# Optimization experiments

Hardware: AMD Instinct MI355X
Metric: run time of the kernel (lower is better)

The kernel has to match this reference:

```python
import jax, jax.numpy as jnp
import numpy as np

DIM = 384
HEADS = 6
POINTS = 4
LEVELS = 3
FFN_DIM = 1024
EPS = 1e-6
SHAPES = [(128, 128), (64, 64), (32, 32)]  # (H, W) per level
B = 4
NQ = 4096


def layer_norm(x, g, b):
    m = jnp.mean(x, axis=-1, keepdims=True)
    v = jnp.mean(jnp.square(x - m), axis=-1, keepdims=True)
    return (x - m) * jax.lax.rsqrt(v + EPS) * g + b


def _bilinear_sample(vl, loc, h, w):
    # vl: [B, heads, Dh, h*w] per-level value; loc: [B, Nq, heads, P, 2] in [0,1]
    # grid_sample(align_corners=False, padding_mode='zeros') semantics
    Bn, Hh, Dh, _ = vl.shape
    Nq, P = loc.shape[1], loc.shape[3]
    x = loc[..., 0] * w - 0.5
    y = loc[..., 1] * h - 0.5
    x0 = jnp.floor(x); y0 = jnp.floor(y)
    wx1 = x - x0; wx0 = 1.0 - wx1
    wy1 = y - y0; wy0 = 1.0 - wy1
    acc = jnp.zeros((Bn, Hh, Dh, Nq, P), dtype=vl.dtype)
    for xi, yi, wgt in ((x0, y0, wx0 * wy0), (x0 + 1, y0, wx1 * wy0),
                        (x0, y0 + 1, wx0 * wy1), (x0 + 1, y0 + 1, wx1 * wy1)):
        valid = (xi >= 0) & (xi <= w - 1) & (yi >= 0) & (yi <= h - 1)
        idx = (jnp.clip(yi, 0, h - 1) * w + jnp.clip(xi, 0, w - 1)).astype(jnp.int32)
        idx = idx.transpose(0, 2, 1, 3).reshape(Bn, Hh, 1, Nq * P)  # [B,heads,1,Nq*P]
        g = jnp.take_along_axis(vl, jnp.broadcast_to(idx, (Bn, Hh, Dh, Nq * P)), axis=3)
        g = g.reshape(Bn, Hh, Dh, Nq, P)
        wm = (wgt * valid.astype(wgt.dtype)).transpose(0, 2, 1, 3)[:, :, None]  # [B,heads,1,Nq,P]
        acc = acc + g * wm
    return acc  # [B, heads, Dh, Nq, P]


def msda(query, value, reference_points, shapes_np, W_off, b_off, W_aw, b_aw, W_v, b_v, W_o, b_o):
    Bn, Nq, D = query.shape
    L = len(shapes_np)
    Dh = D // HEADS
    v = value @ W_v.T + b_v  # [B, Nv, D]
    offsets = (query @ W_off.T + b_off).reshape(Bn, Nq, HEADS, L, POINTS, 2)
    aw = (query @ W_aw.T + b_aw).reshape(Bn, Nq, HEADS, L * POINTS)
    aw = jax.nn.softmax(aw, axis=-1).reshape(Bn, Nq, HEADS, L, POINTS)
    # offset normalizer is [W, H] per level
    norm = jnp.asarray([[w, h] for (h, w) in shapes_np], dtype=query.dtype)
    loc = reference_points[:, :, None, :, None, :] + offsets / norm[None, None, None, :, None, :]
    out = jnp.zeros((Bn, Nq, HEADS, Dh), dtype=query.dtype)
    start = 0
    for l, (h, w) in enumerate(shapes_np):
        vl = v[:, start:start + h * w].reshape(Bn, h * w, HEADS, Dh)
        vl = vl.transpose(0, 2, 3, 1)  # [B, heads, Dh, h*w]
        sampled = _bilinear_sample(vl, loc[:, :, :, l], h, w)  # [B,heads,Dh,Nq,P]
        out = out + jnp.einsum('bhdqp,bqhp->bqhd', sampled, aw[:, :, :, l])
        start += h * w
    return out.reshape(Bn, Nq, D) @ W_o.T + b_o


def setup_inputs():
    key = jax.random.key(0)
    ks = jax.random.split(key, 16)
    nv = sum(h * w for h, w in SHAPES)
    s = 0.02
    f32 = jnp.float32
    return dict(
        query=jax.random.normal(ks[0], (B, NQ, DIM), f32),
        reference_points=jax.random.uniform(ks[1], (B, NQ, LEVELS, 2), f32),
        feat=jax.random.normal(ks[2], (B, nv, DIM), f32),
        spatial_shapes=jnp.asarray(SHAPES, jnp.int32),
        level_start_index=jnp.asarray(np.cumsum([0] + [h * w for h, w in SHAPES])[:-1], jnp.int32),
        qn_g=jnp.ones((DIM,), f32), qn_b=jnp.zeros((DIM,), f32),
        fn_g=jnp.ones((DIM,), f32), fn_b=jnp.zeros((DIM,), f32),
        W_off=jax.random.normal(ks[3], (HEADS * LEVELS * POINTS * 2, DIM), f32) * s,
        b_off=jax.random.normal(ks[4], (HEADS * LEVELS * POINTS * 2,), f32) * s,
        W_aw=jax.random.normal(ks[5], (HEADS * LEVELS * POINTS, DIM), f32) * s,
        b_aw=jnp.zeros((HEADS * LEVELS * POINTS,), f32),
        W_v=jax.random.normal(ks[6], (DIM, DIM), f32) * s, b_v=jnp.zeros((DIM,), f32),
        W_o=jax.random.normal(ks[7], (DIM, DIM), f32) * s, b_o=jnp.zeros((DIM,), f32),
        n1_g=jnp.ones((DIM,), f32), n1_b=jnp.zeros((DIM,), f32),
        W1=jax.random.normal(ks[8], (FFN_DIM, DIM), f32) * s, b1=jnp.zeros((FFN_DIM,), f32),
        W2=jax.random.normal(ks[9], (DIM, FFN_DIM), f32) * s, b2=jnp.zeros((DIM,), f32),
        n2_g=jnp.ones((DIM,), f32), n2_b=jnp.zeros((DIM,), f32),
        gamma=jnp.full((DIM,), 0.01, f32),
    )


def reference(query, reference_points, feat, spatial_shapes, level_start_index,
              qn_g, qn_b, fn_g, fn_b,
              W_off, b_off, W_aw, b_aw, W_v, b_v, W_o, b_o,
              n1_g, n1_b, W1, b1, W2, b2, n2_g, n2_b, gamma):
    shapes_np = [tuple(int(v) for v in row) for row in np.asarray(spatial_shapes)]
    qn = layer_norm(query, qn_g, qn_b)
    fn = layer_norm(feat, fn_g, fn_b)
    # cross_attn (mmcv MSDeformAttn adds identity=query internally, dropout=0)
    x = qn + msda(qn, fn, reference_points, shapes_np,
                  W_off, b_off, W_aw, b_aw, W_v, b_v, W_o, b_o)
    x = layer_norm(x, n1_g, n1_b)
    x = x + (jax.nn.gelu(x @ W1.T + b1) @ W2.T + b2)  # FFN with residual
    x = layer_norm(x, n2_g, n2_b)
    return query + gamma * x
```

## Files before the change

### kernel.cpp

```cpp
#include <hip/hip_runtime.h>
#include <hip/hip_bf16.h>

#define DIMD 384
#define HEADS 6
#define DH 64
#define LEVELS 3
#define POINTS 4
#define FFN 1024
#define BB 4
#define NQ 4096
#define NV 21504
#define MQ (BB*NQ)
#define MV (BB*NV)
#define EPSF 1e-6f

typedef __hip_bfloat16 bf16;
typedef __attribute__((ext_vector_type(8))) short bf16x8;
typedef __attribute__((ext_vector_type(4))) float f32x4;

__device__ __forceinline__ float wave_sum(float v){
  #pragma unroll
  for(int o=32;o;o>>=1) v += __shfl_xor(v,o);
  return v;
}

__global__ __launch_bounds__(256) void prep_k(
  const float* __restrict__ Wv, const float* __restrict__ Wo,
  const float* __restrict__ W1, const float* __restrict__ W2,
  const float* __restrict__ Woff, const float* __restrict__ Waw,
  const float* __restrict__ boff, const float* __restrict__ baw,
  bf16* __restrict__ wv, bf16* __restrict__ wo, bf16* __restrict__ w1,
  bf16* __restrict__ w2, bf16* __restrict__ wcat, float* __restrict__ bcat)
{
  int i = blockIdx.x*256 + threadIdx.x;
  if(i < 147456){ wv[i] = __float2bfloat16(Wv[i]); return; }
  i -= 147456;
  if(i < 147456){ wo[i] = __float2bfloat16(Wo[i]); return; }
  i -= 147456;
  if(i < 393216){ w1[i] = __float2bfloat16(W1[i]); return; }
  i -= 393216;
  if(i < 393216){ w2[i] = __float2bfloat16(W2[i]); return; }
  i -= 393216;
  if(i < 98304){
    int r = i/384, c = i - r*384;
    float v = r<144 ? Woff[r*384+c] : (r<216 ? Waw[(r-144)*384+c] : 0.f);
    wcat[i] = __float2bfloat16(v); return;
  }
  i -= 98304;
  if(i < 256){ bcat[i] = i<144 ? boff[i] : (i<216 ? baw[i-144] : 0.f); }
}

template<int INBF,int OUTBF,int FINAL>
__global__ __launch_bounds__(256) void ln_k(const void* __restrict__ xv,
    const float* __restrict__ g, const float* __restrict__ b,
    const float* __restrict__ q, const float* __restrict__ gamma,
    void* __restrict__ outv, int nrows)
{
  int row = blockIdx.x*4 + (threadIdx.x>>6);
  int lane = threadIdx.x & 63;
  if(row >= nrows) return;
  float vals[6];
  float s=0.f, s2=0.f;
  #pragma unroll
  for(int i=0;i<6;i++){
    float v;
    if constexpr(INBF) v = __bfloat162float(((const bf16*)xv)[(size_t)row*DIMD + lane + i*64]);
    else               v = ((const float*)xv)[(size_t)row*DIMD + lane + i*64];
    vals[i]=v; s += v; s2 += v*v;
  }
  s = wave_sum(s); s2 = wave_sum(s2);
  float m = s*(1.f/DIMD);
  float var = s2*(1.f/DIMD) - m*m;
  float r = rsqrtf(var + EPSF);
  #pragma unroll
  for(int i=0;i<6;i++){
    int k = lane + i*64;
    float t = (vals[i]-m)*r*g[k] + b[k];
    if constexpr(FINAL){
      t = q[(size_t)row*DIMD + k] + gamma[k]*t;
      ((float*)outv)[(size_t)row*DIMD + k] = t;
    } else if constexpr(OUTBF){
      ((bf16*)outv)[(size_t)row*DIMD + k] = __float2bfloat16(t);
    } else {
      ((float*)outv)[(size_t)row*DIMD + k] = t;
    }
  }
}

__global__ __launch_bounds__(512,4) void vgemm_k(
    const bf16* __restrict__ A, const bf16* __restrict__ Bw,
    const float* __restrict__ bias, bf16* __restrict__ out)
{
  __shared__ __align__(16) short As[64*64];
  __shared__ __align__(16) short Bs[384*64];
  const int tid = threadIdx.x;
  const int wid = tid>>6, lane = tid&63;
  const int m0 = blockIdx.x*64;
  f32x4 acc[4][3] = {};
  const int lr8 = lane>>3;
  const int lc8 = (lane&7)*8;

  for(int k0=0; k0<DIMD; k0+=64){
    {
      const bf16* srcA = A + (size_t)(m0 + wid*8 + lr8)*DIMD + k0 + lc8;
      __builtin_amdgcn_global_load_lds((const __attribute__((address_space(1))) void*)srcA,
          (__attribute__((address_space(3))) void*)(As + wid*512), 16, 0, 0);
    }
    #pragma unroll
    for(int u=0;u<6;u++){
      const int t = wid*6 + u;
      const bf16* srcB = Bw + (size_t)(t*8 + lr8)*DIMD + k0 + lc8;
      __builtin_amdgcn_global_load_lds((const __attribute__((address_space(1))) void*)srcB,
          (__attribute__((address_space(3))) void*)(Bs + t*512), 16, 0, 0);
    }
    asm volatile("s_waitcnt vmcnt(0)" ::: "memory");
    __syncthreads();
    #pragma unroll
    for(int ks=0;ks<2;ks++){
      const int cbase = ks*32 + (lane>>4)*8;
      bf16x8 af[4], bfr[3];
      #pragma unroll
      for(int i=0;i<4;i++){
        const int ar = i*16 + (lane&15);
        af[i] = *(const bf16x8*)(As + ar*64 + cbase);
      }
      #pragma unroll
      for(int j=0;j<3;j++){
        const int br = wid*48 + j*16 + (lane&15);
        bfr[j] = *(const bf16x8*)(Bs + br*64 + cbase);
      }
      #pragma unroll
      for(int i=0;i<4;i++)
        #pragma unroll
        for(int j=0;j<3;j++)
          acc[i][j] = __builtin_amdgcn_mfma_f32_16x16x32_bf16(af[i], bfr[j], acc[i][j], 0,0,0);
    }
    __syncthreads();
  }
  #pragma unroll
  for(int i=0;i<4;i++){
    const int r0 = m0 + i*16 + (lane>>4)*4;
    #pragma unroll
    for(int j=0;j<3;j++){
      const int col = wid*48 + j*16 + (lane&15);
      const float bv = bias[col];
      #pragma unroll
      for(int rr=0;rr<4;rr++)
        out[(size_t)(r0+rr)*DIMD + col] = __float2bfloat16(acc[i][j][rr] + bv);
    }
  }
}

template<int GELU_,int STBF,int RES>
__global__ __launch_bounds__(256) void mgemm_k(
    const bf16* __restrict__ A, const bf16* __restrict__ Bw,
    const float* __restrict__ bias, const bf16* __restrict__ res,
    void* __restrict__ Cv, int M, int K, int Nreal, int ldc)
{
  __shared__ __align__(16) short As[128*64];
  __shared__ __align__(16) short Bs[128*64];
  const int tid  = threadIdx.x;
  const int wid  = tid>>6, lane = tid&63;
  const int wr   = wid>>1, wc = wid&1;
  const int m0   = blockIdx.y*128, n0 = blockIdx.x*128;
  f32x4 acc[4][4] = {};

  const int sr = (lane>>3);
  const int sc = (lane&7)*8;

  for(int k0=0; k0<K; k0+=64){
    #pragma unroll
    for(int u=0;u<4;u++){
      const int t = wid*4 + u;
      const int r = t*8 + sr;
      const bf16* srcA = A  + (size_t)(m0+r)*K + k0 + sc;
      const bf16* srcB = Bw + (size_t)(n0+r)*K + k0 + sc;
      __builtin_amdgcn_global_load_lds((const __attribute__((address_space(1))) void*)srcA,
          (__attribute__((address_space(3))) void*)(As + t*512), 16, 0, 0);
      __builtin_amdgcn_global_load_lds((const __attribute__((address_space(1))) void*)srcB,
          (__attribute__((address_space(3))) void*)(Bs + t*512), 16, 0, 0);
    }
    asm volatile("s_waitcnt vmcnt(0)" ::: "memory");
    __syncthreads();
    #pragma unroll
    for(int ks=0;ks<2;ks++){
      bf16x8 af[4], bfr[4];
      #pragma unroll
      for(int i=0;i<4;i++){
        const int ar = wr*64 + i*16 + (lane&15);
        af[i]  = *(const bf16x8*)(As + ar*64 + ks*32 + (lane>>4)*8);
        const int br = wc*64 + i*16 + (lane&15);
        bfr[i] = *(const bf16x8*)(Bs + br*64 + ks*32 + (lane>>4)*8);
      }
      #pragma unroll
      for(int i=0;i<4;i++)
        #pragma unroll
        for(int j=0;j<4;j++)
          acc[i][j] = __builtin_amdgcn_mfma_f32_16x16x32_bf16(af[i], bfr[j], acc[i][j], 0,0,0);
    }
    __syncthreads();
  }
  #pragma unroll
  for(int i=0;i<4;i++){
    const int rbase = m0 + wr*64 + i*16 + (lane>>4)*4;
    #pragma unroll
    for(int j=0;j<4;j++){
      const int col = n0 + wc*64 + j*16 + (lane&15);
      if(col >= Nreal) continue;
      const float bv = bias[col];
      #pragma unroll
      for(int rr=0;rr<4;rr++){
        const int rowg = rbase + rr;
        float v = acc[i][j][rr] + bv;
        if constexpr(RES) v += __bfloat162float(res[(size_t)rowg*ldc + col]);
        if constexpr(GELU_){ float u=v; v = 0.5f*u*(1.f+tanhf(0.7978845608028654f*(u+0.044715f*u*u*u))); }
        if constexpr(STBF) ((bf16*)Cv)[(size_t)rowg*ldc + col] = __float2bfloat16(v);
        else               ((float*)Cv)[(size_t)rowg*ldc + col] = v;
      }
    }
  }
}

__global__ __launch_bounds__(256) void msda_k(
    const bf16* __restrict__ v, const float* __restrict__ offaw,
    const float* __restrict__ refp, const int* __restrict__ sshapes,
    const int* __restrict__ lstart, bf16* __restrict__ out)
{
  __shared__ uint2 plds[8][48];
  const int pid0 = blockIdx.x*8;
  const int tid = threadIdx.x;
  if(tid < 96){
    const int pl = tid/12, p12 = tid - pl*12;
    const int pid = pid0 + pl;
    const int bq = pid/6, h = pid - bq*6;
    const int b  = bq >> 12;
    const float* row = offaw + (size_t)bq*216;
    float mx = -1e30f;
    #pragma unroll
    for(int i=0;i<12;i++) mx = fmaxf(mx, row[144 + h*12 + i]);
    float ssum = 0.f, my = 0.f;
    #pragma unroll
    for(int i=0;i<12;i++){
      const float e = __expf(row[144 + h*12 + i] - mx);
      ssum += e;
      if(i==p12) my = e;
    }
    const float aww = my/ssum;
    const int l = p12>>2, pp = p12&3;
    const int hh = sshapes[2*l], ww = sshapes[2*l+1];
    const int st = lstart[l];
    const float rx = refp[((size_t)bq*LEVELS + l)*2 + 0];
    const float ry = refp[((size_t)bq*LEVELS + l)*2 + 1];
    const float ox = row[(h*12 + p12)*2 + 0];
    const float oy = row[(h*12 + p12)*2 + 1];
    const float px = (rx + ox/(float)ww)*(float)ww - 0.5f;
    const float py = (ry + oy/(float)hh)*(float)hh - 0.5f;
    const float fx0 = floorf(px), fy0 = floorf(py);
    const int x0 = (int)fx0, y0 = (int)fy0;
    const float wx1 = px - fx0, wx0 = 1.f - wx1;
    const float wy1 = py - fy0, wy0 = 1.f - wy1;
    #pragma unroll
    for(int c=0;c<4;c++){
      const int xi = x0 + (c&1);
      const int yi = y0 + (c>>1);
      const float wgt = (c&1 ? wx1 : wx0) * (c>>1 ? wy1 : wy0);
      const bool valid = (xi>=0) & (xi<=ww-1) & (yi>=0) & (yi<=hh-1);
      const int cx = min(max(xi,0), ww-1);
      const int cy = min(max(yi,0), hh-1);
      const unsigned off = (unsigned)((((b*NV + st + cy*ww + cx)*DIMD) + h*DH)*2);
      uint2 pr; pr.x = off; pr.y = __float_as_uint(valid ? wgt*aww : 0.f);
      plds[pl][p12*4 + c] = pr;
    }
  }
  __syncthreads();
  const int pl  = (tid>>5);
  const int pid = pid0 + pl;
  const int ch  = tid & 31;
  const char* vb = (const char*)v;
  float a0 = 0.f, a1 = 0.f;
  #pragma unroll
  for(int c=0;c<48;c++){
    const uint2 pr = plds[pl][c];
    const unsigned g = *(const unsigned*)(vb + pr.x + (ch<<2));
    const float w = __uint_as_float(pr.y);
    a0 = fmaf(w, __uint_as_float(g << 16), a0);
    a1 = fmaf(w, __uint_as_float(g & 0xffff0000u), a1);
  }
  const int bq = pid/6, h = pid - bq*6;
  const unsigned u0 = (unsigned)__builtin_bit_cast(unsigned short, __float2bfloat16(a0));
  const unsigned u1 = (unsigned)__builtin_bit_cast(unsigned short, __float2bfloat16(a1));
  *(unsigned*)((char*)out + (size_t)bq*768 + h*128 + (ch<<2)) = u0 | (u1<<16);
}

static inline size_t rnd(size_t x){ return (x + 511) & ~(size_t)511; }

extern "C" void kernel_launch(void* const* d_in, const int* in_sizes, int n_in,
                              void* d_out, int out_size, void* d_ws, size_t ws_size,
                              hipStream_t stream)
{
  const float* query = (const float*)d_in[0];
  const float* refp  = (const float*)d_in[1];
  const float* feat  = (const float*)d_in[2];
  const int*   sshp  = (const int*)d_in[3];
  const int*   lst   = (const int*)d_in[4];
  const float* qn_g  = (const float*)d_in[5];
  const float* qn_b  = (const float*)d_in[6];
  const float* fn_g  = (const float*)d_in[7];
  const float* fn_b  = (const float*)d_in[8];
  const float* W_off = (const float*)d_in[9];
  const float* b_off = (const float*)d_in[10];
  const float* W_aw  = (const float*)d_in[11];
  const float* b_aw  = (const float*)d_in[12];
  const float* W_v   = (const float*)d_in[13];
  const float* b_v   = (const float*)d_in[14];
  const float* W_o   = (const float*)d_in[15];
  const float* b_o   = (const float*)d_in[16];
  const float* n1_g  = (const float*)d_in[17];
  const float* n1_b  = (const float*)d_in[18];
  const float* W1    = (const float*)d_in[19];
  const float* b1    = (const float*)d_in[20];
  const float* W2    = (const float*)d_in[21];
  const float* b2    = (const float*)d_in[22];
  const float* n2_g  = (const float*)d_in[23];
  const float* n2_b  = (const float*)d_in[24];
  const float* gam   = (const float*)d_in[25];

  char* p = (char*)d_ws;
  bf16* featn = (bf16*)p;
  char* late  = p;
  p += rnd((size_t)MV*DIMD*2);
  bf16* vbuf  = (bf16*)p;  p += rnd((size_t)MV*DIMD*2);
  bf16* qn    = (bf16*)p;  p += rnd((size_t)MQ*DIMD*2);
  bf16* wv    = (bf16*)p;  p += rnd((size_t)147456*2);
  bf16* wo    = (bf16*)p;  p += rnd((size_t)147456*2);
  bf16* w1    = (bf16*)p;  p += rnd((size_t)393216*2);
  bf16* w2    = (bf16*)p;  p += rnd((size_t)393216*2);
  bf16* wcat  = (bf16*)p;  p += rnd((size_t)98304*2);
  float* bcat = (float*)p; p += rnd((size_t)256*4);
  bf16* hbuf  = (bf16*)p;  p += rnd((size_t)MQ*FFN*2);
  bf16* ybuf  = (bf16*)p;  p += rnd((size_t)MQ*DIMD*2);
  char* q2 = late;
  float* offaw = (float*)q2; q2 += rnd((size_t)MQ*216*4);
  bf16*  msda  = (bf16*)q2;  q2 += rnd((size_t)MQ*DIMD*2);
  bf16*  x1    = (bf16*)q2;  q2 += rnd((size_t)MQ*DIMD*2);
  bf16*  x2    = (bf16*)q2;  q2 += rnd((size_t)MQ*DIMD*2);

  prep_k<<<4609, 256, 0, stream>>>(W_v, W_o, W1, W2, W_off, W_aw, b_off, b_aw,
                                   wv, wo, w1, w2, wcat, bcat);
  ln_k<0,1,0><<<MV/4, 256, 0, stream>>>(feat, fn_g, fn_b, nullptr, nullptr, featn, MV);
  ln_k<0,1,0><<<MQ/4, 256, 0, stream>>>(query, qn_g, qn_b, nullptr, nullptr, qn, MQ);
  vgemm_k<<<MV/64, 512, 0, stream>>>(featn, wv, b_v, vbuf);
  mgemm_k<0,0,0><<<dim3(2, MQ/128), 256, 0, stream>>>(qn, wcat, bcat, nullptr, offaw,
                                                      MQ, DIMD, 216, 216);
  msda_k<<<MQ*HEADS/8, 256, 0, stream>>>(vbuf, offaw, refp, sshp, lst, msda);
  mgemm_k<0,1,1><<<dim3(3, MQ/128), 256, 0, stream>>>(msda, wo, b_o, qn, x1,
                                                      MQ, DIMD, DIMD, DIMD);
  ln_k<1,1,0><<<MQ/4, 256, 0, stream>>>(x1, n1_g, n1_b, nullptr, nullptr, x2, MQ);
  mgemm_k<1,1,0><<<dim3(8, MQ/128), 256, 0, stream>>>(x2, w1, b1, nullptr, hbuf,
                                                      MQ, DIMD, FFN, FFN);
  mgemm_k<0,1,1><<<dim3(3, MQ/128), 256, 0, stream>>>(hbuf, w2, b2, x2, ybuf,
                                                      MQ, FFN, DIMD, DIMD);
  ln_k<1,0,1><<<MQ/4, 256, 0, stream>>>(ybuf, n2_g, n2_b, query, gam, (float*)d_out, MQ);
}
```

Baseline: 266.2 us.

## Fuse feature LayerNorm into value-projection GEMM

Replaces the separate LayerNorm pass over the feature map and the value GEMM with one kernel. Each 32-row tile loads its fp32 rows into LDS, normalises them and writes bf16 rows back to LDS, then multiplies by the full 384-column W_v. This avoids writing and re-reading the normalised feature buffer in global memory. In exchange, the tile shrinks to 32 rows with 256 threads and uses about 72KB of dynamic LDS, which lowers occupancy and means W_v is reloaded by twice as many blocks.

Result: slower. 273.2 us (+2.6%).

```diff
diff --git a/kernel.cpp b/kernel.cpp
--- a/kernel.cpp
+++ b/kernel.cpp
@@ -87,29 +87,64 @@
   }
 }
 
-__global__ __launch_bounds__(512,4) void vgemm_k(
-    const bf16* __restrict__ A, const bf16* __restrict__ Bw,
+__global__ __launch_bounds__(256,2) void flnv_k(
+    const float* __restrict__ feat, const float* __restrict__ fg,
+    const float* __restrict__ fb, const bf16* __restrict__ wv,
     const float* __restrict__ bias, bf16* __restrict__ out)
 {
-  __shared__ __align__(16) short As[64*64];
-  __shared__ __align__(16) short Bs[384*64];
+  extern __shared__ char smem[];
+  float* Af = (float*)smem;
+  short* As = (short*)smem;
+  short* Bs = (short*)(smem + 24576);
   const int tid = threadIdx.x;
   const int wid = tid>>6, lane = tid&63;
-  const int m0 = blockIdx.x*64;
-  f32x4 acc[4][3] = {};
-  const int lr8 = lane>>3;
-  const int lc8 = (lane&7)*8;
-
+  const int m0 = blockIdx.x*32;
+
+  #pragma unroll
+  for(int u=0;u<12;u++){
+    const int t = wid*12 + u;
+    const float* src = feat + (size_t)m0*DIMD + t*256 + lane*4;
+    __builtin_amdgcn_global_load_lds((const __attribute__((address_space(1))) void*)src,
+        (__attribute__((address_space(3))) void*)(Af + t*256), 16, 0, 0);
+  }
+  asm volatile("s_waitcnt vmcnt(0)" ::: "memory");
+  __syncthreads();
+
+  {
+    const int r = tid>>3, sub = tid&7;
+    f32x4 va[12];
+    float s=0.f, s2=0.f;
+    #pragma unroll
+    for(int j=0;j<12;j++){
+      va[j] = *(const f32x4*)(Af + r*DIMD + sub*4 + j*32);
+      #pragma unroll
+      for(int e=0;e<4;e++){ s += va[j][e]; s2 += va[j][e]*va[j][e]; }
+    }
+    s  += __shfl_xor(s,1);  s  += __shfl_xor(s,2);  s  += __shfl_xor(s,4);
+    s2 += __shfl_xor(s2,1); s2 += __shfl_xor(s2,2); s2 += __shfl_xor(s2,4);
+    const float m  = s*(1.f/DIMD);
+    const float rs = rsqrtf(s2*(1.f/DIMD) - m*m + EPSF);
+    __syncthreads();
+    #pragma unroll
+    for(int j=0;j<12;j++){
+      const int col = sub*4 + j*32;
+      const f32x4 g4 = *(const f32x4*)(fg + col);
+      const f32x4 b4 = *(const f32x4*)(fb + col);
+      short4 o4;
+      o4.x = __builtin_bit_cast(short, __float2bfloat16((va[j][0]-m)*rs*g4[0] + b4[0]));
+      o4.y = __builtin_bit_cast(short, __float2bfloat16((va[j][1]-m)*rs*g4[1] + b4[1]));
+      o4.z = __builtin_bit_cast(short, __float2bfloat16((va[j][2]-m)*rs*g4[2] + b4[2]));
+      o4.w = __builtin_bit_cast(short, __float2bfloat16((va[j][3]-m)*rs*g4[3] + b4[3]));
+      *(short4*)(As + r*DIMD + col) = o4;
+    }
+  }
+
+  f32x4 acc[2][6] = {};
   for(int k0=0; k0<DIMD; k0+=64){
-    {
-      const bf16* srcA = A + (size_t)(m0 + wid*8 + lr8)*DIMD + k0 + lc8;
-      __builtin_amdgcn_global_load_lds((const __attribute__((address_space(1))) void*)srcA,
-          (__attribute__((address_space(3))) void*)(As + wid*512), 16, 0, 0);
-    }
-    #pragma unroll
-    for(int u=0;u<6;u++){
-      const int t = wid*6 + u;
-      const bf16* srcB = Bw + (size_t)(t*8 + lr8)*DIMD + k0 + lc8;
+    #pragma unroll
+    for(int u=0;u<12;u++){
+      const int t = wid*12 + u;
+      const bf16* srcB = wv + (size_t)(t*8 + (lane>>3))*DIMD + k0 + (lane&7)*8;
       __builtin_amdgcn_global_load_lds((const __attribute__((address_space(1))) void*)srcB,
           (__attribute__((address_space(3))) void*)(Bs + t*512), 16, 0, 0);
     }
@@ -118,31 +153,31 @@
     #pragma unroll
     for(int ks=0;ks<2;ks++){
       const int cbase = ks*32 + (lane>>4)*8;
-      bf16x8 af[4], bfr[3];
-      #pragma unroll
-      for(int i=0;i<4;i++){
+      bf16x8 af[2], bfr[6];
+      #pragma unroll
+      for(int i=0;i<2;i++){
         const int ar = i*16 + (lane&15);
-        af[i] = *(const bf16x8*)(As + ar*64 + cbase);
+        af[i] = *(const bf16x8*)(As + ar*DIMD + k0 + cbase);
       }
       #pragma unroll
-      for(int j=0;j<3;j++){
-        const int br = wid*48 + j*16 + (lane&15);
+      for(int j=0;j<6;j++){
+        const int br = wid*96 + j*16 + (lane&15);
         bfr[j] = *(const bf16x8*)(Bs + br*64 + cbase);
       }
       #pragma unroll
-      for(int i=0;i<4;i++)
+      for(int i=0;i<2;i++)
         #pragma unroll
-        for(int j=0;j<3;j++)
+        for(int j=0;j<6;j++)
           acc[i][j] = __builtin_amdgcn_mfma_f32_16x16x32_bf16(af[i], bfr[j], acc[i][j], 0,0,0);
     }
     __syncthreads();
   }
   #pragma unroll
-  for(int i=0;i<4;i++){
+  for(int i=0;i<2;i++){
     const int r0 = m0 + i*16 + (lane>>4)*4;
     #pragma unroll
-    for(int j=0;j<3;j++){
-      const int col = wid*48 + j*16 + (lane&15);
+    for(int j=0;j<6;j++){
+      const int col = wid*96 + j*16 + (lane&15);
       const float bv = bias[col];
       #pragma unroll
       for(int rr=0;rr<4;rr++)
@@ -246,7 +281,7 @@
       if(i==p12) my = e;
     }
     const float aww = my/ssum;
-    const int l = p12>>2, pp = p12&3;
+    const int l = p12>>2;
     const int hh = sshapes[2*l], ww = sshapes[2*l+1];
     const int st = lstart[l];
     const float rx = refp[((size_t)bq*LEVELS + l)*2 + 0];
@@ -326,9 +361,6 @@
   const float* gam   = (const float*)d_in[25];
 
   char* p = (char*)d_ws;
-  bf16* featn = (bf16*)p;
-  char* late  = p;
-  p += rnd((size_t)MV*DIMD*2);
   bf16* vbuf  = (bf16*)p;  p += rnd((size_t)MV*DIMD*2);
   bf16* qn    = (bf16*)p;  p += rnd((size_t)MQ*DIMD*2);
   bf16* wv    = (bf16*)p;  p += rnd((size_t)147456*2);
@@ -339,17 +371,19 @@
   float* bcat = (float*)p; p += rnd((size_t)256*4);
   bf16* hbuf  = (bf16*)p;  p += rnd((size_t)MQ*FFN*2);
   bf16* ybuf  = (bf16*)p;  p += rnd((size_t)MQ*DIMD*2);
-  char* q2 = late;
-  float* offaw = (float*)q2; q2 += rnd((size_t)MQ*216*4);
-  bf16*  msda  = (bf16*)q2;  q2 += rnd((size_t)MQ*DIMD*2);
-  bf16*  x1    = (bf16*)q2;  q2 += rnd((size_t)MQ*DIMD*2);
-  bf16*  x2    = (bf16*)q2;  q2 += rnd((size_t)MQ*DIMD*2);
+  float* offaw = (float*)p; p += rnd((size_t)MQ*216*4);
+  bf16*  msda  = (bf16*)p;  p += rnd((size_t)MQ*DIMD*2);
+  bf16*  x1    = (bf16*)p;  p += rnd((size_t)MQ*DIMD*2);
+  bf16*  x2    = (bf16*)p;  p += rnd((size_t)MQ*DIMD*2);
+
+  const int FLNV_LDS = 24576 + 384*64*2;
+  hipFuncSetAttribute((const void*)flnv_k,
+                      hipFuncAttributeMaxDynamicSharedMemorySize, FLNV_LDS);
 
   prep_k<<<4609, 256, 0, stream>>>(W_v, W_o, W1, W2, W_off, W_aw, b_off, b_aw,
                                    wv, wo, w1, w2, wcat, bcat);
-  ln_k<0,1,0><<<MV/4, 256, 0, stream>>>(feat, fn_g, fn_b, nullptr, nullptr, featn, MV);
   ln_k<0,1,0><<<MQ/4, 256, 0, stream>>>(query, qn_g, qn_b, nullptr, nullptr, qn, MQ);
-  vgemm_k<<<MV/64, 512, 0, stream>>>(featn, wv, b_v, vbuf);
+  flnv_k<<<MV/32, 256, FLNV_LDS, stream>>>(feat, fn_g, fn_b, wv, b_v, vbuf);
   mgemm_k<0,0,0><<<dim3(2, MQ/128), 256, 0, stream>>>(qn, wcat, bcat, nullptr, offaw,
                                                       MQ, DIMD, 216, 216);
   msda_k<<<MQ*HEADS/8, 256, 0, stream>>>(vbuf, offaw, refp, sshp, lst, msda);
```

## Fuse residual add and LayerNorm into full-row output-projection and FFN2 GEMMs

Applied to the files above, without the earlier changes.

Generalizes the full-width (384-column) vgemm kernel into a templated gl_k that computes whole output rows per block, so the residual add, LayerNorm (via cross-wave shuffle and LDS reduction) and the final gamma-scaled residual can be applied in the GEMM epilogue. This replaces the W_o GEMM plus norm1 and the FFN2 GEMM plus norm2/final kernels with single launches, removing two intermediate bf16 round trips and two LayerNorm passes. In exchange, those GEMMs now run with 64-row tiles at launch bounds (512,2), giving only 256 blocks for M=16384 and possibly lower occupancy and parallelism than the previous 3x128 tiling.

New measurement: 271.3 us. Within noise of the previous version (+1.9%).

```diff
diff --git a/kernel.cpp b/kernel.cpp
--- a/kernel.cpp
+++ b/kernel.cpp
@@ -50,10 +50,9 @@
   if(i < 256){ bcat[i] = i<144 ? boff[i] : (i<216 ? baw[i-144] : 0.f); }
 }
 
-template<int INBF,int OUTBF,int FINAL>
+template<int INBF,int OUTBF>
 __global__ __launch_bounds__(256) void ln_k(const void* __restrict__ xv,
     const float* __restrict__ g, const float* __restrict__ b,
-    const float* __restrict__ q, const float* __restrict__ gamma,
     void* __restrict__ outv, int nrows)
 {
   int row = blockIdx.x*4 + (threadIdx.x>>6);
@@ -76,40 +75,40 @@
   for(int i=0;i<6;i++){
     int k = lane + i*64;
     float t = (vals[i]-m)*r*g[k] + b[k];
-    if constexpr(FINAL){
-      t = q[(size_t)row*DIMD + k] + gamma[k]*t;
-      ((float*)outv)[(size_t)row*DIMD + k] = t;
-    } else if constexpr(OUTBF){
-      ((bf16*)outv)[(size_t)row*DIMD + k] = __float2bfloat16(t);
-    } else {
-      ((float*)outv)[(size_t)row*DIMD + k] = t;
-    }
-  }
-}
-
-__global__ __launch_bounds__(512,4) void vgemm_k(
+    if constexpr(OUTBF) ((bf16*)outv)[(size_t)row*DIMD + k] = __float2bfloat16(t);
+    else                ((float*)outv)[(size_t)row*DIMD + k] = t;
+  }
+}
+
+template<int KK,int MODE>
+__global__ __launch_bounds__(512,2) void gl_k(
     const bf16* __restrict__ A, const bf16* __restrict__ Bw,
-    const float* __restrict__ bias, bf16* __restrict__ out)
+    const float* __restrict__ bias, const bf16* __restrict__ res,
+    const float* __restrict__ g, const float* __restrict__ b,
+    const float* __restrict__ gam, const float* __restrict__ qsrc,
+    void* __restrict__ out)
 {
   __shared__ __align__(16) short As[64*64];
   __shared__ __align__(16) short Bs[384*64];
+  __shared__ float wst[8*64*2];
+  __shared__ float st[64*2];
   const int tid = threadIdx.x;
   const int wid = tid>>6, lane = tid&63;
   const int m0 = blockIdx.x*64;
+  const int lr8 = lane>>3, lc8 = (lane&7)*8;
+  const int cg = lane>>4;
   f32x4 acc[4][3] = {};
-  const int lr8 = lane>>3;
-  const int lc8 = (lane&7)*8;
-
-  for(int k0=0; k0<DIMD; k0+=64){
+
+  for(int k0=0; k0<KK; k0+=64){
     {
-      const bf16* srcA = A + (size_t)(m0 + wid*8 + lr8)*DIMD + k0 + lc8;
+      const bf16* srcA = A + (size_t)(m0 + wid*8 + lr8)*KK + k0 + lc8;
       __builtin_amdgcn_global_load_lds((const __attribute__((address_space(1))) void*)srcA,
           (__attribute__((address_space(3))) void*)(As + wid*512), 16, 0, 0);
     }
     #pragma unroll
     for(int u=0;u<6;u++){
       const int t = wid*6 + u;
-      const bf16* srcB = Bw + (size_t)(t*8 + lr8)*DIMD + k0 + lc8;
+      const bf16* srcB = Bw + (size_t)(t*8 + lr8)*KK + k0 + lc8;
       __builtin_amdgcn_global_load_lds((const __attribute__((address_space(1))) void*)srcB,
           (__attribute__((address_space(3))) void*)(Bs + t*512), 16, 0, 0);
     }
@@ -117,18 +116,14 @@
     __syncthreads();
     #pragma unroll
     for(int ks=0;ks<2;ks++){
-      const int cbase = ks*32 + (lane>>4)*8;
+      const int cbase = ks*32 + cg*8;
       bf16x8 af[4], bfr[3];
       #pragma unroll
-      for(int i=0;i<4;i++){
-        const int ar = i*16 + (lane&15);
-        af[i] = *(const bf16x8*)(As + ar*64 + cbase);
-      }
-      #pragma unroll
-      for(int j=0;j<3;j++){
-        const int br = wid*48 + j*16 + (lane&15);
-        bfr[j] = *(const bf16x8*)(Bs + br*64 + cbase);
-      }
+      for(int i=0;i<4;i++)
+        af[i] = *(const bf16x8*)(As + (i*16 + (lane&15))*64 + cbase);
+      #pragma unroll
+      for(int j=0;j<3;j++)
+        bfr[j] = *(const bf16x8*)(Bs + (wid*48 + j*16 + (lane&15))*64 + cbase);
       #pragma unroll
       for(int i=0;i<4;i++)
         #pragma unroll
@@ -137,25 +132,101 @@
     }
     __syncthreads();
   }
-  #pragma unroll
-  for(int i=0;i<4;i++){
-    const int r0 = m0 + i*16 + (lane>>4)*4;
-    #pragma unroll
-    for(int j=0;j<3;j++){
-      const int col = wid*48 + j*16 + (lane&15);
-      const float bv = bias[col];
-      #pragma unroll
-      for(int rr=0;rr<4;rr++)
-        out[(size_t)(r0+rr)*DIMD + col] = __float2bfloat16(acc[i][j][rr] + bv);
-    }
-  }
-}
-
-template<int GELU_,int STBF,int RES>
+
+  if constexpr(MODE == 0){
+    #pragma unroll
+    for(int i=0;i<4;i++){
+      const int r0 = m0 + i*16 + cg*4;
+      #pragma unroll
+      for(int j=0;j<3;j++){
+        const int col = wid*48 + j*16 + (lane&15);
+        const float bv = bias[col];
+        #pragma unroll
+        for(int rr=0;rr<4;rr++)
+          ((bf16*)out)[(size_t)(r0+rr)*DIMD + col] = __float2bfloat16(acc[i][j][rr] + bv);
+      }
+    }
+    return;
+  } else {
+    float sA[4][4], sB[4][4];
+    #pragma unroll
+    for(int i=0;i<4;i++)
+      #pragma unroll
+      for(int rr=0;rr<4;rr++){ sA[i][rr]=0.f; sB[i][rr]=0.f; }
+    #pragma unroll
+    for(int i=0;i<4;i++){
+      #pragma unroll
+      for(int j=0;j<3;j++){
+        const int col = wid*48 + j*16 + (lane&15);
+        const float bv = bias[col];
+        #pragma unroll
+        for(int rr=0;rr<4;rr++){
+          const int rowg = m0 + i*16 + cg*4 + rr;
+          float v = acc[i][j][rr] + bv
+                  + __bfloat162float(res[(size_t)rowg*DIMD + col]);
+          acc[i][j][rr] = v;
+          sA[i][rr] += v; sB[i][rr] += v*v;
+        }
+      }
+    }
+    #pragma unroll
+    for(int off=1; off<16; off<<=1){
+      #pragma unroll
+      for(int i=0;i<4;i++)
+        #pragma unroll
+        for(int rr=0;rr<4;rr++){
+          sA[i][rr] += __shfl_xor(sA[i][rr], off);
+          sB[i][rr] += __shfl_xor(sB[i][rr], off);
+        }
+    }
+    if((lane&15)==0){
+      #pragma unroll
+      for(int i=0;i<4;i++)
+        #pragma unroll
+        for(int rr=0;rr<4;rr++){
+          const int row = i*16 + cg*4 + rr;
+          wst[(wid*64 + row)*2 + 0] = sA[i][rr];
+          wst[(wid*64 + row)*2 + 1] = sB[i][rr];
+        }
+    }
+    __syncthreads();
+    if(tid < 64){
+      float ms=0.f, m2=0.f;
+      #pragma unroll
+      for(int w=0;w<8;w++){ ms += wst[(w*64+tid)*2]; m2 += wst[(w*64+tid)*2+1]; }
+      const float m  = ms*(1.f/DIMD);
+      const float rs = rsqrtf(m2*(1.f/DIMD) - m*m + EPSF);
+      st[tid*2] = m; st[tid*2+1] = rs;
+    }
+    __syncthreads();
+    #pragma unroll
+    for(int i=0;i<4;i++){
+      #pragma unroll
+      for(int j=0;j<3;j++){
+        const int col = wid*48 + j*16 + (lane&15);
+        const float gc = g[col], bc = b[col];
+        #pragma unroll
+        for(int rr=0;rr<4;rr++){
+          const int row = i*16 + cg*4 + rr;
+          const int rowg = m0 + row;
+          const float t = (acc[i][j][rr] - st[row*2])*st[row*2+1]*gc + bc;
+          if constexpr(MODE == 1){
+            ((bf16*)out)[(size_t)rowg*DIMD + col] = __float2bfloat16(t);
+          } else {
+            ((float*)out)[(size_t)rowg*DIMD + col] =
+                qsrc[(size_t)rowg*DIMD + col] + gam[col]*t;
+          }
+        }
+      }
+    }
+  }
+}
+
+template<int GELU_,int STBF>
 __global__ __launch_bounds__(256) void mgemm_k(
     const bf16* __restrict__ A, const bf16* __restrict__ Bw,
-    const float* __restrict__ bias, const bf16* __restrict__ res,
-    void* __restrict__ Cv, int M, int K, int Nreal, int ldc)
+    const float* __restrict__ bias, void* __restrict__ Cv,
+    int M, int K, int Nreal, int ldc)
 {
   __shared__ __align__(16) short As[128*64];
   __shared__ __align__(16) short Bs[128*64];
@@ -212,7 +283,6 @@
       for(int rr=0;rr<4;rr++){
         const int rowg = rbase + rr;
         float v = acc[i][j][rr] + bv;
-        if constexpr(RES) v += __bfloat162float(res[(size_t)rowg*ldc + col]);
         if constexpr(GELU_){ float u=v; v = 0.5f*u*(1.f+tanhf(0.7978845608028654f*(u+0.044715f*u*u*u))); }
         if constexpr(STBF) ((bf16*)Cv)[(size_t)rowg*ldc + col] = __float2bfloat16(v);
         else               ((float*)Cv)[(size_t)rowg*ldc + col] = v;
@@ -246,7 +316,7 @@
       if(i==p12) my = e;
     }
     const float aww = my/ssum;
-    const int l = p12>>2, pp = p12&3;
+    const int l = p12>>2;
     const int hh = sshapes[2*l], ww = sshapes[2*l+1];
     const int st = lstart[l];
     const float rx = refp[((size_t)bq*LEVELS + l)*2 + 0];
@@ -338,27 +408,24 @@
   bf16* wcat  = (bf16*)p;  p += rnd((size_t)98304*2);
   float* bcat = (float*)p; p += rnd((size_t)256*4);
   bf16* hbuf  = (bf16*)p;  p += rnd((size_t)MQ*FFN*2);
-  bf16* ybuf  = (bf16*)p;  p += rnd((size_t)MQ*DIMD*2);
   char* q2 = late;
   float* offaw = (float*)q2; q2 += rnd((size_t)MQ*216*4);
   bf16*  msda  = (bf16*)q2;  q2 += rnd((size_t)MQ*DIMD*2);
-  bf16*  x1    = (bf16*)q2;  q2 += rnd((size_t)MQ*DIMD*2);
   bf16*  x2    = (bf16*)q2;  q2 += rnd((size_t)MQ*DIMD*2);
 
   prep_k<<<4609, 256, 0, stream>>>(W_v, W_o, W1, W2, W_off, W_aw, b_off, b_aw,
                                    wv, wo, w1, w2, wcat, bcat);
-  ln_k<0,1,0><<<MV/4, 256, 0, stream>>>(feat, fn_g, fn_b, nullptr, nullptr, featn, MV);
-  ln_k<0,1,0><<<MQ/4, 256, 0, stream>>>(query, qn_g, qn_b, nullptr, nullptr, qn, MQ);
-  vgemm_k<<<MV/64, 512, 0, stream>>>(featn, wv, b_v, vbuf);
-  mgemm_k<0,0,0><<<dim3(2, MQ/128), 256, 0, stream>>>(qn, wcat, bcat, nullptr, offaw,
-                                                      MQ, DIMD, 216, 216);
+  ln_k<0,1><<<MV/4, 256, 0, stream>>>(feat, fn_g, fn_b, featn, MV);
+  ln_k<0,1><<<MQ/4, 256, 0, stream>>>(query, qn_g, qn_b, qn, MQ);
+  gl_k<DIMD,0><<<MV/64, 512, 0, stream>>>(featn, wv, b_v, nullptr,
+                                          nullptr, nullptr, nullptr, nullptr, vbuf);
+  mgemm_k<0,0><<<dim3(2, MQ/128), 256, 0, stream>>>(qn, wcat, bcat, offaw,
+                                                    MQ, DIMD, 216, 216);
   msda_k<<<MQ*HEADS/8, 256, 0, stream>>>(vbuf, offaw, refp, sshp, lst, msda);
-  mgemm_k<0,1,1><<<dim3(3, MQ/128), 256, 0, stream>>>(msda, wo, b_o, qn, x1,
-                                                      MQ, DIMD, DIMD, DIMD);
-  ln_k<1,1,0><<<MQ/4, 256, 0, stream>>>(x1, n1_g, n1_b, nullptr, nullptr, x2, MQ);
-  mgemm_k<1,1,0><<<dim3(8, MQ/128), 256, 0, stream>>>(x2, w1, b1, nullptr, hbuf,
-                                                      MQ, DIMD, FFN, FFN);
-  mgemm_k<0,1,1><<<dim3(3, MQ/128), 256, 0, stream>>>(hbuf, w2, b2, x2, ybuf,
-                                                      MQ, FFN, DIMD, DIMD);
-  ln_k<1,0,1><<<MQ/4, 256, 0, stream>>>(ybuf, n2_g, n2_b, query, gam, (float*)d_out, MQ);
-}
+  gl_k<DIMD,1><<<MQ/64, 512, 0, stream>>>(msda, wo, b_o, qn,
+                                          n1_g, n1_b, nullptr, nullptr, x2);
+  mgemm_k<1,1><<<dim3(8, MQ/128), 256, 0, stream>>>(x2, w1, b1, hbuf,
+                                                    MQ, DIMD, FFN, FFN);
+  gl_k<FFN,2><<<MQ/64, 512, 0, stream>>>(hbuf, w2, b2, x2,
+                                         n2_g, n2_b, gam, query, (float*)d_out);
+}
```
